# Performance work log

Hardware: AMD Instinct MI355X
Metric: run time of the kernel (lower is better)

Reference implementation:

```python
import jax, jax.numpy as jnp
import numpy as np

N, E, B = 50000, 800000, 512
DIN, H, G, M = 128, 128, 32, 128
EPS = 1e-5


def _gcn_layer(h, src, dst, W, b):
    h = h @ W  # [N, H]
    loop = jnp.arange(N)
    s = jnp.concatenate([src, loop])
    d = jnp.concatenate([dst, loop])
    deg = jax.ops.segment_sum(jnp.ones(s.shape, h.dtype), d, num_segments=N)
    dinv = jax.lax.rsqrt(jnp.maximum(deg, 1.0))  # deg >= 1 due to self-loops
    norm = dinv[s] * dinv[d]  # [E+N]
    out = jax.ops.segment_sum(norm[:, None] * h[s], d, num_segments=N)
    return out + b


def _bn_relu(h, gamma, beta):
    mu = jnp.mean(h, axis=0)
    var = jnp.mean((h - mu) ** 2, axis=0)
    return jax.nn.relu((h - mu) * jax.lax.rsqrt(var + EPS) * gamma + beta)


def setup_inputs() -> dict:
    key = jax.random.key(0)
    ks = jax.random.split(key, 20)
    inp = {
        "x": jax.random.normal(ks[0], (N, DIN), jnp.float32),
        "edge_index": jax.random.randint(ks[1], (2, E), 0, N),
        "batch": jnp.sort(jax.random.randint(ks[2], (N,), 0, B)),
        "global_feats": jax.random.normal(ks[3], (B, G), jnp.float32),
    }
    dims = [DIN, H, H]
    for i in range(3):
        inp[f"W{i}"] = jax.random.normal(ks[4 + i], (dims[i], H), jnp.float32) / np.sqrt(dims[i])
        inp[f"b{i}"] = jnp.zeros((H,), jnp.float32)
        inp[f"g{i}"] = jnp.ones((H,), jnp.float32)
        inp[f"be{i}"] = jnp.zeros((H,), jnp.float32)
    inp["M1w"] = jax.random.normal(ks[10], (H + G, M), jnp.float32) / np.sqrt(H + G)
    inp["M1b"] = jnp.zeros((M,), jnp.float32)
    inp["M2w"] = jax.random.normal(ks[11], (M, M // 2), jnp.float32) / np.sqrt(M)
    inp["M2b"] = jnp.zeros((M // 2,), jnp.float32)
    inp["M3w"] = jax.random.normal(ks[12], (M // 2, 1), jnp.float32) / np.sqrt(M // 2)
    inp["M3b"] = jnp.zeros((1,), jnp.float32)
    return inp


def reference(x, edge_index, batch, global_feats,
              W0, b0, g0, be0, W1, b1, g1, be1, W2, b2, g2, be2,
              M1w, M1b, M2w, M2b, M3w, M3b):
    src, dst = edge_index[0], edge_index[1]
    h = x
    for W, b, g, be in ((W0, b0, g0, be0), (W1, b1, g1, be1), (W2, b2, g2, be2)):
        h = _bn_relu(_gcn_layer(h, src, dst, W, b), g, be)
    # global mean pool over graphs
    sums = jax.ops.segment_sum(h, batch, num_segments=B)  # [B, H]
    cnt = jax.ops.segment_sum(jnp.ones((N,), h.dtype), batch, num_segments=B)
    pooled = sums / jnp.maximum(cnt, 1.0)[:, None]
    z = jnp.concatenate([pooled, global_feats], axis=1)  # [B, H+G]
    z = jax.nn.relu(z @ M1w + M1b)
    z = jax.nn.relu(z @ M2w + M2b)
    out = z @ M3w + M3b  # [B, 1]
    return out.reshape(-1)
```

## Files before the change

### kernel.cpp

```cpp
#include <hip/hip_runtime.h>

#define NN 50000
#define NE 800000
#define BG 512
#define HD 128
#define GD 32
#define MD 128
#define EPSV 1e-5f
#define NBK 256
#define BSTR 196
#define BCAP 4096
#define SP 136
#define CSB 128

typedef __attribute__((ext_vector_type(8))) short bf16x8;
typedef __attribute__((ext_vector_type(4))) float f32x4;

static __device__ __forceinline__ unsigned short f2bf(float f) {
    unsigned int u = __float_as_uint(f);
    u += 0x7fffu + ((u >> 16) & 1u);
    return (unsigned short)(u >> 16);
}
static __device__ __forceinline__ float bfu(unsigned short v) {
    return __uint_as_float((unsigned int)v << 16);
}
static __device__ __forceinline__ float bf_lo(unsigned int v) {
    return __uint_as_float(v << 16);
}
static __device__ __forceinline__ float bf_hi(unsigned int v) {
    return __uint_as_float(v & 0xffff0000u);
}

__global__ __launch_bounds__(256) void k_bin(const int* __restrict__ src,
                                             const int* __restrict__ dst,
                                             int* __restrict__ bucket_cnt,
                                             unsigned int* __restrict__ binned) {
    __shared__ int hcnt[NBK];
    __shared__ int hbase[NBK];
    int tid = threadIdx.x;
    int e0 = blockIdx.x * 2048;
    unsigned int pv[8];
    int bk[8], rk[8];
#pragma unroll
    for (int i = 0; i < 8; ++i) {
        int e = e0 + i * 256 + tid;
        if (e < NE) {
            int s = src[e];
            int d = dst[e];
            bk[i] = d / BSTR;
            pv[i] = ((unsigned int)(d - bk[i] * BSTR) << 16) | (unsigned int)s;
        } else {
            bk[i] = -1;
        }
    }
    hcnt[tid] = 0;
    __syncthreads();
#pragma unroll
    for (int i = 0; i < 8; ++i)
        if (bk[i] >= 0) rk[i] = atomicAdd(&hcnt[bk[i]], 1);
    __syncthreads();
    hbase[tid] = atomicAdd(&bucket_cnt[tid], hcnt[tid]);
    __syncthreads();
#pragma unroll
    for (int i = 0; i < 8; ++i)
        if (bk[i] >= 0)
            binned[(size_t)bk[i] * BCAP + hbase[bk[i]] + rk[i]] = pv[i];
}

__global__ __launch_bounds__(256) void k_csr(const unsigned int* __restrict__ binned,
                                             const int* __restrict__ bucket_cnt,
                                             int* __restrict__ offsets,
                                             float* __restrict__ dinv,
                                             int* __restrict__ csr,
                                             const float* __restrict__ W0,
                                             const float* __restrict__ W1,
                                             const float* __restrict__ W2,
                                             unsigned short* __restrict__ Wt) {
    __shared__ unsigned short sW[128 * 130];
    __shared__ int ls[256];
    __shared__ int h[BSTR];
    __shared__ int cur[BSTR];
    __shared__ int bpre_s;
    int b = blockIdx.x, t = threadIdx.x;
    if (b >= NBK) {
        const float* Wsrc = (b == NBK) ? W0 : ((b == NBK + 1) ? W1 : W2);
#pragma unroll
        for (int i = 0; i < 64; ++i) {
            int idx = i * 256 + t;
            int k = idx >> 7, n = idx & 127;
            sW[n * 130 + k] = f2bf(Wsrc[idx]);
        }
        __syncthreads();
        unsigned short* o = Wt + (size_t)(b - NBK) * 16384;
#pragma unroll
        for (int i = 0; i < 64; ++i) {
            int idx = i * 256 + t;
            int n = idx >> 7, k = idx & 127;
            o[idx] = sW[n * 130 + k];
        }
        return;
    }
    int bc = bucket_cnt[t];
    ls[t] = bc;
    __syncthreads();
    for (int off = 1; off < 256; off <<= 1) {
        int c0 = ls[t];
        int add = (t >= off) ? ls[t - off] : 0;
        __syncthreads();
        ls[t] = c0 + add;
        __syncthreads();
    }
    if (t == b) bpre_s = ls[t] - bc;
    if (t < BSTR) h[t] = 0;
    __syncthreads();
    int bpre = bpre_s;
    int nb = bucket_cnt[b];
    const unsigned int* base = binned + (size_t)b * BCAP;
    for (int e = t; e < nb; e += 256)
        atomicAdd(&h[base[e] >> 16], 1);
    __syncthreads();
    int c = (t < BSTR) ? h[t] : 0;
    ls[t] = c;
    __syncthreads();
    for (int off = 1; off < 256; off <<= 1) {
        int c0 = ls[t];
        int add = (t >= off) ? ls[t - off] : 0;
        __syncthreads();
        ls[t] = c0 + add;
        __syncthreads();
    }
    int node = b * BSTR + t;
    if (t < BSTR) {
        int excl = ls[t] - c + bpre;
        cur[t] = excl;
        if (node < NN) {
            offsets[node] = excl;
            dinv[node] = rsqrtf((float)(c + 1));
            if (node == NN - 1) offsets[NN] = NE;
        }
    }
    __syncthreads();
    for (int e = t; e < nb; e += 256) {
        unsigned int v = base[e];
        int pos = atomicAdd(&cur[v >> 16], 1);
        csr[pos] = (int)(v & 0xffffu);
    }
}

__global__ __launch_bounds__(256) void k_gemm(const float* __restrict__ Inf,
                                              const unsigned short* __restrict__ Inh,
                                              const unsigned short* __restrict__ Wt,
                                              unsigned short* __restrict__ Th,
                                              const float* __restrict__ stats,
                                              const float* __restrict__ gamma,
                                              const float* __restrict__ beta,
                                              const float* __restrict__ dinv,
                                              int useBN) {
    __shared__ unsigned short Abf[64 * SP];
    __shared__ unsigned short WtL[128 * SP];
    __shared__ float ssS[256];
    int tid = threadIdx.x;
    int rowBase = blockIdx.x * 64;
    if (useBN) {
        ssS[tid] = stats[tid];
        __syncthreads();
        if (tid < 128) {
            float mu = ssS[tid] * (1.f / NN);
            float var = ssS[128 + tid] * (1.f / NN) - mu * mu;
            float sc = gamma[tid] * rsqrtf(var + EPSV);
            float sh = beta[tid] - mu * sc;
            ssS[tid] = sc;
            ssS[128 + tid] = sh;
        }
        __syncthreads();
#pragma unroll
        for (int i = 0; i < 4; ++i) {
            int q = tid + i * 256;
            int row = q >> 4;
            int k8 = (q & 15) * 8;
            int rg = rowBase + row;
            if (rg >= NN) rg = NN - 1;
            bf16x8 raw = *(const bf16x8*)&Inh[(size_t)rg * HD + k8];
            unsigned short o[8];
#pragma unroll
            for (int e = 0; e < 8; ++e) {
                float v = bfu((unsigned short)raw[e]);
                v = fmaxf(v * ssS[k8 + e] + ssS[128 + k8 + e], 0.f);
                o[e] = f2bf(v);
            }
            *(bf16x8*)&Abf[row * SP + k8] = *(bf16x8*)o;
        }
    } else {
#pragma unroll
        for (int i = 0; i < 8; ++i) {
            int q = tid + i * 256;
            int row = q >> 5;
            int c4 = (q & 31) * 4;
            int rg = rowBase + row;
            if (rg >= NN) rg = NN - 1;
            float4 v = *(const float4*)&Inf[(size_t)rg * HD + c4];
            unsigned short* p = &Abf[row * SP + c4];
            p[0] = f2bf(v.x); p[1] = f2bf(v.y); p[2] = f2bf(v.z); p[3] = f2bf(v.w);
        }
    }
#pragma unroll
    for (int i = 0; i < 8; ++i) {
        int q = tid + i * 256;
        int n = q >> 4;
        int k8 = (q & 15) * 8;
        bf16x8 w = *(const bf16x8*)&Wt[n * HD + k8];
        *(bf16x8*)&WtL[n * SP + k8] = w;
    }
    __syncthreads();
    int lane = tid & 63;
    int wv = tid >> 6;
    int quad = lane >> 4;
    int lrow = wv * 16 + (lane & 15);
    f32x4 acc[8];
#pragma unroll
    for (int c = 0; c < 8; ++c) acc[c] = (f32x4){0.f, 0.f, 0.f, 0.f};
#pragma unroll
    for (int qk = 0; qk < 4; ++qk) {
        int ko = quad * 8 + qk * 32;
        bf16x8 bfr = *(const bf16x8*)&Abf[lrow * SP + ko];
#pragma unroll
        for (int c = 0; c < 8; ++c) {
            bf16x8 afr = *(const bf16x8*)&WtL[(c * 16 + (lane & 15)) * SP + ko];
            acc[c] = __builtin_amdgcn_mfma_f32_16x16x32_bf16(afr, bfr, acc[c], 0, 0, 0);
        }
    }
    int grow = rowBase + lrow;
    if (grow < NN) {
        float di = dinv[grow];
#pragma unroll
        for (int c = 0; c < 8; ++c) {
            ushort4 o;
            o.x = f2bf(acc[c][0] * di);
            o.y = f2bf(acc[c][1] * di);
            o.z = f2bf(acc[c][2] * di);
            o.w = f2bf(acc[c][3] * di);
            *(ushort4*)&Th[(size_t)grow * HD + c * 16 + quad * 4] = o;
        }
    }
}

__global__ __launch_bounds__(256, 8) void k_aggregate(const uint2* __restrict__ T2,
                                                      const int* __restrict__ offsets,
                                                      const int* __restrict__ csr,
                                                      const float* __restrict__ dinv,
                                                      const float* __restrict__ bias,
                                                      unsigned short* __restrict__ Ah) {
    int d = blockIdx.x * 4 + (threadIdx.x >> 6);
    int l = threadIdx.x & 63;
    int half = l >> 5;
    int li = l & 31;
    if (d >= NN) return;
    int start = offsets[d], end = offsets[d + 1];
    float a0 = 0.f, a1 = 0.f, a2 = 0.f, a3 = 0.f;
    int j = start;
    for (; j + 15 < end; j += 16) {
        int s[8];
        uint2 v[8];
#pragma unroll
        for (int i = 0; i < 8; ++i) s[i] = csr[j + 2 * i + half];
#pragma unroll
        for (int i = 0; i < 8; ++i) v[i] = T2[(size_t)s[i] * 32 + li];
#pragma unroll
        for (int i = 0; i < 8; ++i) {
            a0 += bf_lo(v[i].x); a1 += bf_hi(v[i].x);
            a2 += bf_lo(v[i].y); a3 += bf_hi(v[i].y);
        }
    }
    for (; j + 7 < end; j += 8) {
        int s0 = csr[j + half];
        int s1 = csr[j + 2 + half];
        int s2 = csr[j + 4 + half];
        int s3 = csr[j + 6 + half];
        uint2 v0 = T2[(size_t)s0 * 32 + li];
        uint2 v1 = T2[(size_t)s1 * 32 + li];
        uint2 v2 = T2[(size_t)s2 * 32 + li];
        uint2 v3 = T2[(size_t)s3 * 32 + li];
        a0 += bf_lo(v0.x); a1 += bf_hi(v0.x); a2 += bf_lo(v0.y); a3 += bf_hi(v0.y);
        a0 += bf_lo(v1.x); a1 += bf_hi(v1.x); a2 += bf_lo(v1.y); a3 += bf_hi(v1.y);
        a0 += bf_lo(v2.x); a1 += bf_hi(v2.x); a2 += bf_lo(v2.y); a3 += bf_hi(v2.y);
        a0 += bf_lo(v3.x); a1 += bf_hi(v3.x); a2 += bf_lo(v3.y); a3 += bf_hi(v3.y);
    }
    for (; j + 1 < end; j += 2) {
        int s0 = csr[j + half];
        uint2 v0 = T2[(size_t)s0 * 32 + li];
        a0 += bf_lo(v0.x); a1 += bf_hi(v0.x); a2 += bf_lo(v0.y); a3 += bf_hi(v0.y);
    }
    if (j < end && half == 0) {
        int s0 = csr[j];
        uint2 v0 = T2[(size_t)s0 * 32 + li];
        a0 += bf_lo(v0.x); a1 += bf_hi(v0.x); a2 += bf_lo(v0.y); a3 += bf_hi(v0.y);
    }
    a0 += __shfl_xor(a0, 32);
    a1 += __shfl_xor(a1, 32);
    a2 += __shfl_xor(a2, 32);
    a3 += __shfl_xor(a3, 32);
    if (half == 0) {
        float di = dinv[d];
        uint2 vd = T2[(size_t)d * 32 + li];
        float4 bs = *(const float4*)&bias[4 * li];
        ushort4 o;
        o.x = f2bf(di * (a0 + bf_lo(vd.x)) + bs.x);
        o.y = f2bf(di * (a1 + bf_hi(vd.x)) + bs.y);
        o.z = f2bf(di * (a2 + bf_lo(vd.y)) + bs.z);
        o.w = f2bf(di * (a3 + bf_hi(vd.y)) + bs.w);
        *(ushort4*)&Ah[(size_t)d * HD + 4 * li] = o;
    }
}

__global__ __launch_bounds__(256) void k_colstats(const uint2* __restrict__ A2,
                                                  float* __restrict__ stats) {
    int li = threadIdx.x & 31;
    int rr = threadIdx.x >> 5;
    float4 s = {0.f, 0.f, 0.f, 0.f}, q = {0.f, 0.f, 0.f, 0.f};
    for (int row = blockIdx.x * 8 + rr; row < NN; row += CSB * 8) {
        uint2 u = A2[(size_t)row * 32 + li];
        float x0 = bf_lo(u.x), x1 = bf_hi(u.x), x2 = bf_lo(u.y), x3 = bf_hi(u.y);
        s.x += x0; s.y += x1; s.z += x2; s.w += x3;
        q.x += x0 * x0; q.y += x1 * x1; q.z += x2 * x2; q.w += x3 * x3;
    }
    __shared__ float4 lsum[256], lqum[256];
    lsum[threadIdx.x] = s;
    lqum[threadIdx.x] = q;
    __syncthreads();
    if (rr == 0) {
        float4 a = lsum[li];
#pragma unroll
        for (int g = 1; g < 8; ++g) {
            float4 b = lsum[g * 32 + li];
            a.x += b.x; a.y += b.y; a.z += b.z; a.w += b.w;
        }
        atomicAdd(&stats[4 * li + 0], a.x);
        atomicAdd(&stats[4 * li + 1], a.y);
        atomicAdd(&stats[4 * li + 2], a.z);
        atomicAdd(&stats[4 * li + 3], a.w);
    } else if (rr == 1) {
        float4 a = lqum[li];
#pragma unroll
        for (int g = 1; g < 8; ++g) {
            float4 b = lqum[g * 32 + li];
            a.x += b.x; a.y += b.y; a.z += b.z; a.w += b.w;
        }
        atomicAdd(&stats[128 + 4 * li + 0], a.x);
        atomicAdd(&stats[128 + 4 * li + 1], a.y);
        atomicAdd(&stats[128 + 4 * li + 2], a.z);
        atomicAdd(&stats[128 + 4 * li + 3], a.w);
    }
}

__global__ __launch_bounds__(256) void k_pool(const unsigned int* __restrict__ Au,
                                              const int* __restrict__ batch,
                                              const float* __restrict__ stats,
                                              const float* __restrict__ gamma,
                                              const float* __restrict__ beta,
                                              float* __restrict__ pooled) {
    __shared__ float ssP[256];
    int t = threadIdx.x;
    ssP[t] = stats[t];
    __syncthreads();
    if (t < 128) {
        float mu = ssP[t] * (1.f / NN);
        float var = ssP[128 + t] * (1.f / NN) - mu * mu;
        float sc = gamma[t] * rsqrtf(var + EPSV);
        float sh = beta[t] - mu * sc;
        ssP[t] = sc;
        ssP[128 + t] = sh;
    }
    __syncthreads();
    int fu = t & 63;
    int half = t >> 6;
    int r0 = blockIdx.x * 64;
    int rend = min(r0 + 64, NN);
    float s0 = ssP[2 * fu], s1 = ssP[2 * fu + 1];
    float h0 = ssP[128 + 2 * fu], h1 = ssP[128 + 2 * fu + 1];
    float a0 = 0.f, a1 = 0.f;
    int cg = -1;
    for (int r = r0 + half; r < rend; r += 4) {
        int g = batch[r];
        if (g != cg) {
            if (cg >= 0) {
                atomicAdd(&pooled[(size_t)cg * HD + 2 * fu], a0);
                atomicAdd(&pooled[(size_t)cg * HD + 2 * fu + 1], a1);
            }
            cg = g;
            a0 = 0.f; a1 = 0.f;
        }
        unsigned int v = Au[(size_t)r * 64 + fu];
        a0 += fmaxf(bf_lo(v) * s0 + h0, 0.f);
        a1 += fmaxf(bf_hi(v) * s1 + h1, 0.f);
    }
    if (cg >= 0) {
        atomicAdd(&pooled[(size_t)cg * HD + 2 * fu], a0);
        atomicAdd(&pooled[(size_t)cg * HD + 2 * fu + 1], a1);
    }
}

__global__ __launch_bounds__(128) void k_mlp(const float* __restrict__ pooled,
                                             const int* __restrict__ batch,
                                             const float* __restrict__ gfeat,
                                             const float* __restrict__ M1w,
                                             const float* __restrict__ M1b,
                                             const float* __restrict__ M2w,
                                             const float* __restrict__ M2b,
                                             const float* __restrict__ M3w,
                                             const float* __restrict__ M3b,
                                             float* __restrict__ out) {
    __shared__ int sb[2];
    __shared__ float z[HD + GD];
    __shared__ float z1[MD];
    __shared__ float z2[MD / 2];
    int b = blockIdx.x, t = threadIdx.x;
    if (t < 2) {
        int val = b + t;
        int lo = 0, hi = NN;
        while (lo < hi) {
            int mid = (lo + hi) >> 1;
            if (batch[mid] < val) lo = mid + 1; else hi = mid;
        }
        sb[t] = lo;
    }
    __syncthreads();
    float ic = 1.f / fmaxf((float)(sb[1] - sb[0]), 1.f);
    z[t] = pooled[(size_t)b * HD + t] * ic;
    if (t < GD) z[HD + t] = gfeat[b * GD + t];
    __syncthreads();
    float a = M1b[t];
    for (int k = 0; k < HD + GD; ++k) a += z[k] * M1w[k * MD + t];
    z1[t] = fmaxf(a, 0.f);
    __syncthreads();
    if (t < MD / 2) {
        float a2 = M2b[t];
        for (int k = 0; k < MD; ++k) a2 += z1[k] * M2w[k * (MD / 2) + t];
        z2[t] = fmaxf(a2, 0.f);
    }
    __syncthreads();
    if (t < 64) {
        float p = z2[t] * M3w[t];
#pragma unroll
        for (int off = 32; off; off >>= 1) p += __shfl_down(p, off);
        if (t == 0) out[b] = p + M3b[0];
    }
}

static inline size_t alg(size_t x) { return (x + 255) & ~(size_t)255; }

extern "C" void kernel_launch(void* const* d_in, const int* in_sizes, int n_in,
                              void* d_out, int out_size, void* d_ws, size_t ws_size,
                              hipStream_t stream) {
    const float* x = (const float*)d_in[0];
    const int* ei = (const int*)d_in[1];
    const int* batch = (const int*)d_in[2];
    const float* gf = (const float*)d_in[3];
    const float* W[3] = {(const float*)d_in[4], (const float*)d_in[8], (const float*)d_in[12]};
    const float* bb[3] = {(const float*)d_in[5], (const float*)d_in[9], (const float*)d_in[13]};
    const float* gg[3] = {(const float*)d_in[6], (const float*)d_in[10], (const float*)d_in[14]};
    const float* be[3] = {(const float*)d_in[7], (const float*)d_in[11], (const float*)d_in[15]};
    const float* M1w = (const float*)d_in[16];
    const float* M1b = (const float*)d_in[17];
    const float* M2w = (const float*)d_in[18];
    const float* M2b = (const float*)d_in[19];
    const float* M3w = (const float*)d_in[20];
    const float* M3b = (const float*)d_in[21];
    float* out = (float*)d_out;

    char* w = (char*)d_ws;
    int* bucket_cnt = (int*)w;    w += alg((size_t)NBK * 4);
    float* pooled = (float*)w;    w += alg((size_t)BG * HD * 4);
    float* stats = (float*)w;     w += alg((size_t)3 * 256 * 4);
    size_t zspan = (size_t)(w - (char*)d_ws);
    int* offsets = (int*)w;       w += alg((size_t)(NN + 1) * 4);
    int* csr = (int*)w;           w += alg((size_t)NE * 4);
    float* dinv = (float*)w;      w += alg((size_t)NN * 4);
    unsigned short* Wt = (unsigned short*)w;  w += alg((size_t)3 * 16384 * 2);
    unsigned int* binned = (unsigned int*)w;  w += alg((size_t)NBK * BCAP * 4);
    unsigned short* Ah = (unsigned short*)w;  w += alg((size_t)NN * HD * 2);
    unsigned short* Th = (unsigned short*)w;  w += alg((size_t)NN * HD * 2);

    const int* src = ei;
    const int* dst = ei + NE;

    hipMemsetAsync(bucket_cnt, 0, zspan, stream);
    k_bin<<<(NE + 2047) / 2048, 256, 0, stream>>>(src, dst, bucket_cnt, binned);
    k_csr<<<NBK + 3, 256, 0, stream>>>(binned, bucket_cnt, offsets, dinv, csr,
                                       W[0], W[1], W[2], Wt);

    for (int L = 0; L < 3; ++L) {
        k_gemm<<<(NN + 63) / 64, 256, 0, stream>>>(x, Ah, Wt + (size_t)L * 16384, Th,
                                                   stats + (L ? (L - 1) * 256 : 0),
                                                   gg[L ? L - 1 : 0], be[L ? L - 1 : 0],
                                                   dinv, L > 0);
        k_aggregate<<<(NN + 3) / 4, 256, 0, stream>>>((const uint2*)Th, offsets, csr,
                                                      dinv, bb[L], Ah);
        k_colstats<<<CSB, 256, 0, stream>>>((const uint2*)Ah, stats + L * 256);
    }

    k_pool<<<(NN + 63) / 64, 256, 0, stream>>>((const unsigned int*)Ah, batch,
                                               stats + 2 * 256, gg[2], be[2], pooled);
    k_mlp<<<BG, 128, 0, stream>>>(pooled, batch, gf, M1w, M1b, M2w, M2b, M3w, M3b, out);
}
```

Measured before the change: 374.3 us.

## Fuse whole GCN pipeline into one persistent kernel with grid barriers

Replaces the sequence of about a dozen launches (bin, csr, per-layer gemm/aggregate/colstats, pool, mlp) with one persistent 512-block kernel. Phases are separated by a software grid barrier built on atomics, and work is striped over virtual block indices. The column statistics are now accumulated inside the aggregation pass, which removes a separate read of the activations. The memset becomes a small init kernel. The cost is that each barrier is a spin-wait and the grid is limited to 512 blocks at 2 blocks per CU, which may cut occupancy for the memory-bound aggregation phase. Correctness also depends on all 512 blocks being resident at the same time.

Result: slower. 1.124 ms (+200.3%).

```diff
diff --git a/kernel.cpp b/kernel.cpp
--- a/kernel.cpp
+++ b/kernel.cpp
@@ -11,7 +11,12 @@
 #define BSTR 196
 #define BCAP 4096
 #define SP 136
-#define CSB 128
+#define GRID 512
+#define BINB 391
+#define GEMMV 782
+#define AGGV 12500
+#define POOLV 782
+#define SMEMB 53248
 
 typedef __attribute__((ext_vector_type(8))) short bf16x8;
 typedef __attribute__((ext_vector_type(4))) float f32x4;
@@ -31,15 +36,41 @@
     return __uint_as_float(v & 0xffff0000u);
 }
 
-__global__ __launch_bounds__(256) void k_bin(const int* __restrict__ src,
-                                             const int* __restrict__ dst,
-                                             int* __restrict__ bucket_cnt,
-                                             unsigned int* __restrict__ binned) {
-    __shared__ int hcnt[NBK];
-    __shared__ int hbase[NBK];
+__global__ __launch_bounds__(256) void k_init(int* bucket_cnt, float* pooled,
+                                              float* stats, unsigned* bar) {
+    int idx = blockIdx.x * 256 + threadIdx.x;
+    if (idx < NBK) bucket_cnt[idx] = 0;
+    if (idx < BG * HD) pooled[idx] = 0.f;
+    if (idx < 768) stats[idx] = 0.f;
+    if (idx < 2) bar[idx] = 0u;
+}
+
+static __device__ __forceinline__ void gsync(unsigned* bar) {
+    __syncthreads();
+    if (threadIdx.x == 0) {
+        __threadfence();
+        unsigned g = __hip_atomic_load(&bar[1], __ATOMIC_RELAXED, __HIP_MEMORY_SCOPE_AGENT);
+        unsigned a = __hip_atomic_fetch_add(&bar[0], 1u, __ATOMIC_ACQ_REL, __HIP_MEMORY_SCOPE_AGENT);
+        if (a == GRID - 1) {
+            __hip_atomic_store(&bar[0], 0u, __ATOMIC_RELAXED, __HIP_MEMORY_SCOPE_AGENT);
+            __hip_atomic_store(&bar[1], g + 1u, __ATOMIC_RELEASE, __HIP_MEMORY_SCOPE_AGENT);
+        } else {
+            while (__hip_atomic_load(&bar[1], __ATOMIC_RELAXED, __HIP_MEMORY_SCOPE_AGENT) == g)
+                __builtin_amdgcn_s_sleep(4);
+        }
+        __threadfence();
+    }
+    __syncthreads();
+}
+
+static __device__ __forceinline__ void bin_body(int vb, const int* src, const int* dst,
+                                                int* bucket_cnt, unsigned* binned,
+                                                char* smem) {
+    int* hcnt = (int*)smem;
+    int* hbase = (int*)(smem + 1024);
     int tid = threadIdx.x;
-    int e0 = blockIdx.x * 2048;
-    unsigned int pv[8];
+    int e0 = vb * 2048;
+    unsigned pv[8];
     int bk[8], rk[8];
 #pragma unroll
     for (int i = 0; i < 8; ++i) {
@@ -48,7 +79,7 @@
             int s = src[e];
             int d = dst[e];
             bk[i] = d / BSTR;
-            pv[i] = ((unsigned int)(d - bk[i] * BSTR) << 16) | (unsigned int)s;
+            pv[i] = ((unsigned)(d - bk[i] * BSTR) << 16) | (unsigned)s;
         } else {
             bk[i] = -1;
         }
@@ -67,22 +98,15 @@
             binned[(size_t)bk[i] * BCAP + hbase[bk[i]] + rk[i]] = pv[i];
 }
 
-__global__ __launch_bounds__(256) void k_csr(const unsigned int* __restrict__ binned,
-                                             const int* __restrict__ bucket_cnt,
-                                             int* __restrict__ offsets,
-                                             float* __restrict__ dinv,
-                                             int* __restrict__ csr,
-                                             const float* __restrict__ W0,
-                                             const float* __restrict__ W1,
-                                             const float* __restrict__ W2,
-                                             unsigned short* __restrict__ Wt) {
-    __shared__ unsigned short sW[128 * 130];
-    __shared__ int ls[256];
-    __shared__ int h[BSTR];
-    __shared__ int cur[BSTR];
-    __shared__ int bpre_s;
-    int b = blockIdx.x, t = threadIdx.x;
+static __device__ __forceinline__ void csr_body(int b, const unsigned* binned,
+                                                const int* bucket_cnt, int* offsets,
+                                                float* dinv, int* csr,
+                                                const float* W0, const float* W1,
+                                                const float* W2, unsigned short* Wt,
+                                                char* smem) {
+    int t = threadIdx.x;
     if (b >= NBK) {
+        unsigned short* sW = (unsigned short*)smem;
         const float* Wsrc = (b == NBK) ? W0 : ((b == NBK + 1) ? W1 : W2);
 #pragma unroll
         for (int i = 0; i < 64; ++i) {
@@ -100,6 +124,10 @@
         }
         return;
     }
+    int* ls = (int*)(smem + 33280);
+    int* h = ls + 256;
+    int* cur = h + BSTR;
+    int* bpre = cur + BSTR;
     int bc = bucket_cnt[t];
     ls[t] = bc;
     __syncthreads();
@@ -110,12 +138,12 @@
         ls[t] = c0 + add;
         __syncthreads();
     }
-    if (t == b) bpre_s = ls[t] - bc;
+    if (t == b) bpre[0] = ls[t] - bc;
     if (t < BSTR) h[t] = 0;
     __syncthreads();
-    int bpre = bpre_s;
+    int bpre_v = bpre[0];
     int nb = bucket_cnt[b];
-    const unsigned int* base = binned + (size_t)b * BCAP;
+    const unsigned* base = binned + (size_t)b * BCAP;
     for (int e = t; e < nb; e += 256)
         atomicAdd(&h[base[e] >> 16], 1);
     __syncthreads();
@@ -131,7 +159,7 @@
     }
     int node = b * BSTR + t;
     if (t < BSTR) {
-        int excl = ls[t] - c + bpre;
+        int excl = ls[t] - c + bpre_v;
         cur[t] = excl;
         if (node < NN) {
             offsets[node] = excl;
@@ -141,26 +169,25 @@
     }
     __syncthreads();
     for (int e = t; e < nb; e += 256) {
-        unsigned int v = base[e];
+        unsigned v = base[e];
         int pos = atomicAdd(&cur[v >> 16], 1);
         csr[pos] = (int)(v & 0xffffu);
     }
 }
 
-__global__ __launch_bounds__(256) void k_gemm(const float* __restrict__ Inf,
-                                              const unsigned short* __restrict__ Inh,
-                                              const unsigned short* __restrict__ Wt,
-                                              unsigned short* __restrict__ Th,
-                                              const float* __restrict__ stats,
-                                              const float* __restrict__ gamma,
-                                              const float* __restrict__ beta,
-                                              const float* __restrict__ dinv,
-                                              int useBN) {
-    __shared__ unsigned short Abf[64 * SP];
-    __shared__ unsigned short WtL[128 * SP];
-    __shared__ float ssS[256];
+static __device__ __forceinline__ void gemm_body(int vb, const float* Inf,
+                                                 const unsigned short* Inh,
+                                                 const unsigned short* Wtg,
+                                                 unsigned short* Th, const float* stats,
+                                                 const float* gamma, const float* beta,
+                                                 const float* dinv, int useBN,
+                                                 char* smem) {
+    unsigned short* Abf = (unsigned short*)smem;
+    unsigned short* WtL = (unsigned short*)(smem + 64 * SP * 2);
+    float* ssS = (float*)(smem + 64 * SP * 2 + 128 * SP * 2);
     int tid = threadIdx.x;
-    int rowBase = blockIdx.x * 64;
+    int rowBase = vb * 64;
+    __syncthreads();
     if (useBN) {
         ssS[tid] = stats[tid];
         __syncthreads();
@@ -208,7 +235,7 @@
         int q = tid + i * 256;
         int n = q >> 4;
         int k8 = (q & 15) * 8;
-        bf16x8 w = *(const bf16x8*)&Wt[n * HD + k8];
+        bf16x8 w = *(const bf16x8*)&Wtg[n * HD + k8];
         *(bf16x8*)&WtL[n * SP + k8] = w;
     }
     __syncthreads();
@@ -244,13 +271,11 @@
     }
 }
 
-__global__ __launch_bounds__(256, 8) void k_aggregate(const uint2* __restrict__ T2,
-                                                      const int* __restrict__ offsets,
-                                                      const int* __restrict__ csr,
-                                                      const float* __restrict__ dinv,
-                                                      const float* __restrict__ bias,
-                                                      unsigned short* __restrict__ Ah) {
-    int d = blockIdx.x * 4 + (threadIdx.x >> 6);
+static __device__ __forceinline__ void agg_body(int vb, const uint2* T2,
+                                                const int* offsets, const int* csr,
+                                                const float* dinv, const float* bias,
+                                                unsigned short* Ah, f32x4& s4, f32x4& q4) {
+    int d = vb * 4 + (threadIdx.x >> 6);
     int l = threadIdx.x & 63;
     int half = l >> 5;
     int li = l & 31;
@@ -303,117 +328,29 @@
         float di = dinv[d];
         uint2 vd = T2[(size_t)d * 32 + li];
         float4 bs = *(const float4*)&bias[4 * li];
+        float v0 = di * (a0 + bf_lo(vd.x)) + bs.x;
+        float v1 = di * (a1 + bf_hi(vd.x)) + bs.y;
+        float v2 = di * (a2 + bf_lo(vd.y)) + bs.z;
+        float v3 = di * (a3 + bf_hi(vd.y)) + bs.w;
+        s4[0] += v0; s4[1] += v1; s4[2] += v2; s4[3] += v3;
+        q4[0] += v0 * v0; q4[1] += v1 * v1; q4[2] += v2 * v2; q4[3] += v3 * v3;
         ushort4 o;
-        o.x = f2bf(di * (a0 + bf_lo(vd.x)) + bs.x);
-        o.y = f2bf(di * (a1 + bf_hi(vd.x)) + bs.y);
-        o.z = f2bf(di * (a2 + bf_lo(vd.y)) + bs.z);
-        o.w = f2bf(di * (a3 + bf_hi(vd.y)) + bs.w);
+        o.x = f2bf(v0); o.y = f2bf(v1); o.z = f2bf(v2); o.w = f2bf(v3);
         *(ushort4*)&Ah[(size_t)d * HD + 4 * li] = o;
     }
 }
 
-__global__ __launch_bounds__(256) void k_colstats(const uint2* __restrict__ A2,
-                                                  float* __restrict__ stats) {
-    int li = threadIdx.x & 31;
-    int rr = threadIdx.x >> 5;
-    float4 s = {0.f, 0.f, 0.f, 0.f}, q = {0.f, 0.f, 0.f, 0.f};
-    for (int row = blockIdx.x * 8 + rr; row < NN; row += CSB * 8) {
-        uint2 u = A2[(size_t)row * 32 + li];
-        float x0 = bf_lo(u.x), x1 = bf_hi(u.x), x2 = bf_lo(u.y), x3 = bf_hi(u.y);
-        s.x += x0; s.y += x1; s.z += x2; s.w += x3;
-        q.x += x0 * x0; q.y += x1 * x1; q.z += x2 * x2; q.w += x3 * x3;
-    }
-    __shared__ float4 lsum[256], lqum[256];
-    lsum[threadIdx.x] = s;
-    lqum[threadIdx.x] = q;
-    __syncthreads();
-    if (rr == 0) {
-        float4 a = lsum[li];
-#pragma unroll
-        for (int g = 1; g < 8; ++g) {
-            float4 b = lsum[g * 32 + li];
-            a.x += b.x; a.y += b.y; a.z += b.z; a.w += b.w;
-        }
-        atomicAdd(&stats[4 * li + 0], a.x);
-        atomicAdd(&stats[4 * li + 1], a.y);
-        atomicAdd(&stats[4 * li + 2], a.z);
-        atomicAdd(&stats[4 * li + 3], a.w);
-    } else if (rr == 1) {
-        float4 a = lqum[li];
-#pragma unroll
-        for (int g = 1; g < 8; ++g) {
-            float4 b = lqum[g * 32 + li];
-            a.x += b.x; a.y += b.y; a.z += b.z; a.w += b.w;
-        }
-        atomicAdd(&stats[128 + 4 * li + 0], a.x);
-        atomicAdd(&stats[128 + 4 * li + 1], a.y);
-        atomicAdd(&stats[128 + 4 * li + 2], a.z);
-        atomicAdd(&stats[128 + 4 * li + 3], a.w);
-    }
-}
-
-__global__ __launch_bounds__(256) void k_pool(const unsigned int* __restrict__ Au,
-                                              const int* __restrict__ batch,
-                                              const float* __restrict__ stats,
-                                              const float* __restrict__ gamma,
-                                              const float* __restrict__ beta,
-                                              float* __restrict__ pooled) {
-    __shared__ float ssP[256];
+static __device__ __forceinline__ void mlp_body(int b, const float* pooled,
+                                                const int* batch, const float* gfeat,
+                                                const float* M1w, const float* M1b,
+                                                const float* M2w, const float* M2b,
+                                                const float* M3w, const float* M3b,
+                                                float* out, char* smem) {
+    int* sb = (int*)smem;
+    float* z = (float*)(smem + 16);
+    float* z1 = z + HD + GD;
+    float* z2 = z1 + MD;
     int t = threadIdx.x;
-    ssP[t] = stats[t];
-    __syncthreads();
-    if (t < 128) {
-        float mu = ssP[t] * (1.f / NN);
-        float var = ssP[128 + t] * (1.f / NN) - mu * mu;
-        float sc = gamma[t] * rsqrtf(var + EPSV);
-        float sh = beta[t] - mu * sc;
-        ssP[t] = sc;
-        ssP[128 + t] = sh;
-    }
-    __syncthreads();
-    int fu = t & 63;
-    int half = t >> 6;
-    int r0 = blockIdx.x * 64;
-    int rend = min(r0 + 64, NN);
-    float s0 = ssP[2 * fu], s1 = ssP[2 * fu + 1];
-    float h0 = ssP[128 + 2 * fu], h1 = ssP[128 + 2 * fu + 1];
-    float a0 = 0.f, a1 = 0.f;
-    int cg = -1;
-    for (int r = r0 + half; r < rend; r += 4) {
-        int g = batch[r];
-        if (g != cg) {
-            if (cg >= 0) {
-                atomicAdd(&pooled[(size_t)cg * HD + 2 * fu], a0);
-                atomicAdd(&pooled[(size_t)cg * HD + 2 * fu + 1], a1);
-            }
-            cg = g;
-            a0 = 0.f; a1 = 0.f;
-        }
-        unsigned int v = Au[(size_t)r * 64 + fu];
-        a0 += fmaxf(bf_lo(v) * s0 + h0, 0.f);
-        a1 += fmaxf(bf_hi(v) * s1 + h1, 0.f);
-    }
-    if (cg >= 0) {
-        atomicAdd(&pooled[(size_t)cg * HD + 2 * fu], a0);
-        atomicAdd(&pooled[(size_t)cg * HD + 2 * fu + 1], a1);
-    }
-}
-
-__global__ __launch_bounds__(128) void k_mlp(const float* __restrict__ pooled,
-                                             const int* __restrict__ batch,
-                                             const float* __restrict__ gfeat,
-                                             const float* __restrict__ M1w,
-                                             const float* __restrict__ M1b,
-                                             const float* __restrict__ M2w,
-                                             const float* __restrict__ M2b,
-                                             const float* __restrict__ M3w,
-                                             const float* __restrict__ M3b,
-                                             float* __restrict__ out) {
-    __shared__ int sb[2];
-    __shared__ float z[HD + GD];
-    __shared__ float z1[MD];
-    __shared__ float z2[MD / 2];
-    int b = blockIdx.x, t = threadIdx.x;
     if (t < 2) {
         int val = b + t;
         int lo = 0, hi = NN;
@@ -425,12 +362,14 @@
     }
     __syncthreads();
     float ic = 1.f / fmaxf((float)(sb[1] - sb[0]), 1.f);
-    z[t] = pooled[(size_t)b * HD + t] * ic;
-    if (t < GD) z[HD + t] = gfeat[b * GD + t];
-    __syncthreads();
-    float a = M1b[t];
-    for (int k = 0; k < HD + GD; ++k) a += z[k] * M1w[k * MD + t];
-    z1[t] = fmaxf(a, 0.f);
+    if (t < HD) z[t] = pooled[(size_t)b * HD + t] * ic;
+    else if (t < HD + GD) z[t] = gfeat[b * GD + (t - HD)];
+    __syncthreads();
+    if (t < MD) {
+        float a = M1b[t];
+        for (int k = 0; k < HD + GD; ++k) a += z[k] * M1w[k * MD + t];
+        z1[t] = fmaxf(a, 0.f);
+    }
     __syncthreads();
     if (t < MD / 2) {
         float a2 = M2b[t];
@@ -444,6 +383,124 @@
         for (int off = 32; off; off >>= 1) p += __shfl_down(p, off);
         if (t == 0) out[b] = p + M3b[0];
     }
+}
+
+__global__ __launch_bounds__(256, 2) void k_mega(
+    const float* __restrict__ x, const int* __restrict__ src, const int* __restrict__ dst,
+    const int* __restrict__ batch, const float* __restrict__ gfeat,
+    const float* __restrict__ W0, const float* __restrict__ W1, const float* __restrict__ W2,
+    const float* __restrict__ b0, const float* __restrict__ b1, const float* __restrict__ b2,
+    const float* __restrict__ g0, const float* __restrict__ g1, const float* __restrict__ g2,
+    const float* __restrict__ be0, const float* __restrict__ be1, const float* __restrict__ be2,
+    const float* __restrict__ M1w, const float* __restrict__ M1b,
+    const float* __restrict__ M2w, const float* __restrict__ M2b,
+    const float* __restrict__ M3w, const float* __restrict__ M3b,
+    float* __restrict__ out,
+    int* bucket_cnt, float* pooled, float* stats,
+    int* offsets, int* csr, float* dinv,
+    unsigned short* Wt, unsigned* binned,
+    unsigned short* Ah, unsigned short* Th, unsigned* bar) {
+    __shared__ __align__(16) char smem[SMEMB];
+    int bx = blockIdx.x;
+
+    if (bx < BINB) bin_body(bx, src, dst, bucket_cnt, binned, smem);
+    gsync(bar);
+
+    if (bx < NBK + 3)
+        csr_body(bx, binned, bucket_cnt, offsets, dinv, csr, W0, W1, W2, Wt, smem);
+    gsync(bar);
+
+    const uint2* T2 = (const uint2*)Th;
+#pragma unroll
+    for (int L = 0; L < 3; ++L) {
+        const unsigned short* WtgL = Wt + (size_t)L * 16384;
+        const float* stIn = (L == 0) ? stats : stats + (L - 1) * 256;
+        const float* gIn = (L == 1) ? g0 : g1;
+        const float* beIn = (L == 1) ? be0 : be1;
+        for (int vb = bx; vb < GEMMV; vb += GRID)
+            gemm_body(vb, x, Ah, WtgL, Th, stIn, gIn, beIn, dinv, L > 0, smem);
+        gsync(bar);
+        {
+            const float* biasL = (L == 0) ? b0 : ((L == 1) ? b1 : b2);
+            float* statsL = stats + L * 256;
+            f32x4 s4 = {0.f, 0.f, 0.f, 0.f}, q4 = {0.f, 0.f, 0.f, 0.f};
+            for (int vb = bx; vb < AGGV; vb += GRID)
+                agg_body(vb, T2, offsets, csr, dinv, biasL, Ah, s4, q4);
+            float4* lsum = (float4*)smem;
+            float4* lq = (float4*)(smem + 4096);
+            __syncthreads();
+            float4 ws; ws.x = s4[0]; ws.y = s4[1]; ws.z = s4[2]; ws.w = s4[3];
+            float4 wq; wq.x = q4[0]; wq.y = q4[1]; wq.z = q4[2]; wq.w = q4[3];
+            lsum[threadIdx.x] = ws;
+            lq[threadIdx.x] = wq;
+            __syncthreads();
+            int t = threadIdx.x;
+            if (t < 32) {
+                float4 a = lsum[t], bb_ = lsum[64 + t], cc = lsum[128 + t], dd = lsum[192 + t];
+                atomicAdd(&statsL[4 * t + 0], a.x + bb_.x + cc.x + dd.x);
+                atomicAdd(&statsL[4 * t + 1], a.y + bb_.y + cc.y + dd.y);
+                atomicAdd(&statsL[4 * t + 2], a.z + bb_.z + cc.z + dd.z);
+                atomicAdd(&statsL[4 * t + 3], a.w + bb_.w + cc.w + dd.w);
+            } else if (t >= 64 && t < 96) {
+                int u = t - 64;
+                float4 a = lq[u], bb_ = lq[64 + u], cc = lq[128 + u], dd = lq[192 + u];
+                atomicAdd(&statsL[128 + 4 * u + 0], a.x + bb_.x + cc.x + dd.x);
+                atomicAdd(&statsL[128 + 4 * u + 1], a.y + bb_.y + cc.y + dd.y);
+                atomicAdd(&statsL[128 + 4 * u + 2], a.z + bb_.z + cc.z + dd.z);
+                atomicAdd(&statsL[128 + 4 * u + 3], a.w + bb_.w + cc.w + dd.w);
+            }
+        }
+        gsync(bar);
+    }
+
+    {
+        float* ssP = (float*)smem;
+        int t = threadIdx.x;
+        ssP[t] = stats[512 + t];
+        __syncthreads();
+        if (t < 128) {
+            float mu = ssP[t] * (1.f / NN);
+            float var = ssP[128 + t] * (1.f / NN) - mu * mu;
+            float sc = g2[t] * rsqrtf(var + EPSV);
+            float sh = be2[t] - mu * sc;
+            ssP[t] = sc;
+            ssP[128 + t] = sh;
+        }
+        __syncthreads();
+        int fu = t & 63;
+        int half = t >> 6;
+        float s0 = ssP[2 * fu], s1 = ssP[2 * fu + 1];
+        float h0 = ssP[128 + 2 * fu], h1 = ssP[128 + 2 * fu + 1];
+        const unsigned* Au = (const unsigned*)Ah;
+        for (int vb = bx; vb < POOLV; vb += GRID) {
+            int r0 = vb * 64;
+            int rend = min(r0 + 64, NN);
+            float a0 = 0.f, a1 = 0.f;
+            int cg = -1;
+            for (int r = r0 + half; r < rend; r += 4) {
+                int g = batch[r];
+                if (g != cg) {
+                    if (cg >= 0) {
+                        atomicAdd(&pooled[(size_t)cg * HD + 2 * fu], a0);
+                        atomicAdd(&pooled[(size_t)cg * HD + 2 * fu + 1], a1);
+                    }
+                    cg = g;
+                    a0 = 0.f; a1 = 0.f;
+                }
+                unsigned v = Au[(size_t)r * 64 + fu];
+                a0 += fmaxf(bf_lo(v) * s0 + h0, 0.f);
+                a1 += fmaxf(bf_hi(v) * s1 + h1, 0.f);
+            }
+            if (cg >= 0) {
+                atomicAdd(&pooled[(size_t)cg * HD + 2 * fu], a0);
+                atomicAdd(&pooled[(size_t)cg * HD + 2 * fu + 1], a1);
+            }
+        }
+    }
+    gsync(bar);
+
+    if (bx < BG)
+        mlp_body(bx, pooled, batch, gfeat, M1w, M1b, M2w, M2b, M3w, M3b, out, smem);
 }
 
 static inline size_t alg(size_t x) { return (x + 255) & ~(size_t)255; }
@@ -471,34 +528,23 @@
     int* bucket_cnt = (int*)w;    w += alg((size_t)NBK * 4);
     float* pooled = (float*)w;    w += alg((size_t)BG * HD * 4);
     float* stats = (float*)w;     w += alg((size_t)3 * 256 * 4);
-    size_t zspan = (size_t)(w - (char*)d_ws);
+    unsigned* bar = (unsigned*)w; w += alg((size_t)64);
     int* offsets = (int*)w;       w += alg((size_t)(NN + 1) * 4);
     int* csr = (int*)w;           w += alg((size_t)NE * 4);
     float* dinv = (float*)w;      w += alg((size_t)NN * 4);
     unsigned short* Wt = (unsigned short*)w;  w += alg((size_t)3 * 16384 * 2);
-    unsigned int* binned = (unsigned int*)w;  w += alg((size_t)NBK * BCAP * 4);
+    unsigned* binned = (unsigned*)w;          w += alg((size_t)NBK * BCAP * 4);
     unsigned short* Ah = (unsigned short*)w;  w += alg((size_t)NN * HD * 2);
     unsigned short* Th = (unsigned short*)w;  w += alg((size_t)NN * HD * 2);
 
     const int* src = ei;
     const int* dst = ei + NE;
 
-    hipMemsetAsync(bucket_cnt, 0, zspan, stream);
-    k_bin<<<(NE + 2047) / 2048, 256, 0, stream>>>(src, dst, bucket_cnt, binned);
-    k_csr<<<NBK + 3, 256, 0, stream>>>(binned, bucket_cnt, offsets, dinv, csr,
-                                       W[0], W[1], W[2], Wt);
-
-    for (int L = 0; L < 3; ++L) {
-        k_gemm<<<(NN + 63) / 64, 256, 0, stream>>>(x, Ah, Wt + (size_t)L * 16384, Th,
-                                                   stats + (L ? (L - 1) * 256 : 0),
-                                                   gg[L ? L - 1 : 0], be[L ? L - 1 : 0],
-                                                   dinv, L > 0);
-        k_aggregate<<<(NN + 3) / 4, 256, 0, stream>>>((const uint2*)Th, offsets, csr,
-                                                      dinv, bb[L], Ah);
-        k_colstats<<<CSB, 256, 0, stream>>>((const uint2*)Ah, stats + L * 256);
-    }
-
-    k_pool<<<(NN + 63) / 64, 256, 0, stream>>>((const unsigned int*)Ah, batch,
-                                               stats + 2 * 256, gg[2], be[2], pooled);
-    k_mlp<<<BG, 128, 0, stream>>>(pooled, batch, gf, M1w, M1b, M2w, M2b, M3w, M3b, out);
-}
+    k_init<<<256, 256, 0, stream>>>(bucket_cnt, pooled, stats, bar);
+    k_mega<<<GRID, 256, 0, stream>>>(x, src, dst, batch, gf,
+                                     W[0], W[1], W[2], bb[0], bb[1], bb[2],
+                                     gg[0], gg[1], gg[2], be[0], be[1], be[2],
+                                     M1w, M1b, M2w, M2b, M3w, M3b, out,
+                                     bucket_cnt, pooled, stats, offsets, csr, dinv,
+                                     Wt, binned, Ah, Th, bar);
+}
```
